# Kernel optimization log

Measured on AMD Instinct MI355X. Metric: run time of the kernel, lower is better.

Reference implementation:

```python
import jax, jax.numpy as jnp
import numpy as np

K = 512
DIM = 256
BETA = 0.25


def setup_inputs() -> dict:
    key = jax.random.key(0)
    k1, k2 = jax.random.split(key)
    x = jax.random.normal(k1, (64, DIM, 32, 32), dtype=jnp.float32)
    lookup_table = jax.random.normal(k2, (K, DIM), dtype=jnp.float32)
    return {"x": x, "lookup_table": lookup_table}


def reference(x, lookup_table):
    b, d, h, w = x.shape
    # [b,d,h,w] -> [b*h*w, d]
    xf = jnp.transpose(x, (0, 2, 3, 1)).reshape(-1, d)
    # Squared Euclidean distances (argmin identical to torch.cdist argmin)
    d2 = (
        jnp.sum(xf * xf, axis=-1, keepdims=True)
        - 2.0 * (xf @ lookup_table.T)
        + jnp.sum(lookup_table * lookup_table, axis=-1)
    )  # [N, K]
    q = jnp.argmin(d2, axis=1)  # [N]
    x_e = lookup_table[q].reshape(b, h, w, d).transpose(0, 3, 1, 2)  # [b,d,h,w]
    q_x = q.reshape(b, h, w)
    codebook_loss = jnp.mean(jnp.square(jax.lax.stop_gradient(x) - x_e))
    commitment_loss = jnp.mean(jnp.square(x - jax.lax.stop_gradient(x_e)))
    loss = codebook_loss + BETA * commitment_loss
    return x_e, q_x, loss
```

## Files before the change

kernel.cpp:

```cpp
#include <hip/hip_runtime.h>

#define DIM     256
#define HW      1024
#define N_ROWS  65536
#define QBM     32
#define NBLK    2048
#define MARGIN  0.125f
#define MARGIN3 0.1875f

#define OUT_Q_OFF    16777216
#define OUT_LOSS_OFF 16842752

#define WS_DIST    512
#define WS_X2      2560
#define WS_CNTF_I  4608
#define WS_CNTP_I  4609
#define WS_LISTF_I 5120
#define WS_LISTP_I 21504
#define CAP_F      16384
#define CAP_P      32768
#define WS_LUTH_B  786432

typedef _Float16 half8v __attribute__((ext_vector_type(8)));
typedef float floatx4 __attribute__((ext_vector_type(4)));

__global__ void c2_kernel(const float* __restrict__ lut, float* __restrict__ ws) {
    if (threadIdx.x == 0) { ((int*)ws)[WS_CNTF_I] = 0; ((int*)ws)[WS_CNTP_I] = 0; }
    int t = threadIdx.x;
    for (int k = t; k < 512; k += 256) {
        const float4* row = (const float4*)(lut + (size_t)k * DIM);
        float s = 0.f;
        #pragma unroll 8
        for (int i = 0; i < DIM / 4; ++i) {
            float4 v = row[i];
            s += v.x * v.x + v.y * v.y + v.z * v.z + v.w * v.w;
        }
        ws[k] = s;
    }
}

__global__ void lutprep_kernel(const float* __restrict__ lut, float* __restrict__ ws) {
    int g = blockIdx.x * 256 + threadIdx.x;
    int lane = g & 63;
    int ctu  = (g >> 6) & 31;
    int dcg  = g >> 11;
    int code = ctu * 16 + (lane & 15);
    int d0   = dcg * 32 + (lane >> 4) * 8;
    const float* src = lut + (size_t)code * DIM + d0;
    half8v h;
    #pragma unroll
    for (int j = 0; j < 8; ++j) h[j] = (_Float16)src[j];
    char* dst = (char*)ws + WS_LUTH_B + (size_t)(dcg * 32 + ctu) * 1024 + lane * 16;
    *(half8v*)dst = h;
}

#define MERGE_TRIPLE(v1,i1,v2,i2,v3, w1,j1,w2,j2,w3)                          \
    {                                                                         \
        float a1,a2,a3,b1v,b2v; int a1i,a2i,b1i,b2i;                          \
        bool bf = (w1 < v1) || (w1 == v1 && j1 < i1);                         \
        if (bf) { a1=w1;a1i=j1;a2=w2;a2i=j2;a3=w3; b1v=v1;b1i=i1;b2v=v2;b2i=i2; } \
        else    { a1=v1;a1i=i1;a2=v2;a2i=i2;a3=v3; b1v=w1;b1i=j1;b2v=w2;b2i=j2; } \
        bool sa = (a2 < b1v) || (a2 == b1v && a2i < b1i);                     \
        v1 = a1; i1 = a1i;                                                    \
        if (sa) { v2 = a2; i2 = a2i; v3 = fminf(a3, b1v); }                   \
        else    { v2 = b1v; i2 = b1i; v3 = fminf(a2, b2v); }                  \
    }

#define CTU_BODY(CUR, NXT, CTU, DO_PREFETCH)                                          \
    {                                                                                 \
        if (DO_PREFETCH) {                                                            \
            _Pragma("unroll")                                                         \
            for (int dc = 0; dc < 8; ++dc)                                            \
                NXT[dc] = *(const half8v*)(luth + (size_t)(dc * 32 + (CTU) + 1) * 1024 + lane * 16); \
        }                                                                             \
        floatx4 acc00 = (floatx4)0.f, acc01 = (floatx4)0.f;                           \
        floatx4 acc10 = (floatx4)0.f, acc11 = (floatx4)0.f;                           \
        _Pragma("unroll")                                                             \
        for (int dc = 0; dc < 4; ++dc) {                                              \
            acc00 = __builtin_amdgcn_mfma_f32_16x16x32_f16(a[0][dc], CUR[dc], acc00, 0, 0, 0); \
            acc10 = __builtin_amdgcn_mfma_f32_16x16x32_f16(a[1][dc], CUR[dc], acc10, 0, 0, 0); \
        }                                                                             \
        _Pragma("unroll")                                                             \
        for (int dc = 4; dc < 8; ++dc) {                                              \
            acc01 = __builtin_amdgcn_mfma_f32_16x16x32_f16(a[0][dc], CUR[dc], acc01, 0, 0, 0); \
            acc11 = __builtin_amdgcn_mfma_f32_16x16x32_f16(a[1][dc], CUR[dc], acc11, 0, 0, 0); \
        }                                                                             \
        float c2v = ws[(CTU) * 16 + l15];                                             \
        int code = (CTU) * 16 + l15;                                                  \
        _Pragma("unroll")                                                             \
        for (int r = 0; r < 4; ++r) {                                                 \
            float d0f = fmaf(-2.f, acc00[r] + acc01[r], c2v);                         \
            if (d0f < v1[0][r])      { v3[0][r]=v2[0][r]; v2[0][r]=v1[0][r]; i2[0][r]=i1[0][r]; v1[0][r]=d0f; i1[0][r]=code; } \
            else if (d0f < v2[0][r]) { v3[0][r]=v2[0][r]; v2[0][r]=d0f; i2[0][r]=code; } \
            else if (d0f < v3[0][r]) { v3[0][r]=d0f; }                                \
            float d1f = fmaf(-2.f, acc10[r] + acc11[r], c2v);                         \
            if (d1f < v1[1][r])      { v3[1][r]=v2[1][r]; v2[1][r]=v1[1][r]; i2[1][r]=i1[1][r]; v1[1][r]=d1f; i1[1][r]=code; } \
            else if (d1f < v2[1][r]) { v3[1][r]=v2[1][r]; v2[1][r]=d1f; i2[1][r]=code; } \
            else if (d1f < v3[1][r]) { v3[1][r]=d1f; }                                \
        }                                                                             \
    }

__global__ __launch_bounds__(64, 2) void vq_kernel(const float* __restrict__ x,
                                                   const float* __restrict__ lut,
                                                   float* __restrict__ out,
                                                   float* __restrict__ ws) {
    __shared__ int qsh[QBM];
    const char* luth = (const char*)ws + WS_LUTH_B;

    const int lane = threadIdx.x;
    const int blk  = blockIdx.x;
    const int n0   = blk * QBM;
    const int b    = n0 >> 10;
    const int hw0  = n0 & 1023;
    const float* xb = x + (size_t)b * (DIM * HW) + hw0;

    const int l15 = lane & 15;
    const int l4  = lane >> 4;

    half8v a[2][8];
    float x2local = 0.f;
    #pragma unroll
    for (int rt = 0; rt < 2; ++rt) {
        #pragma unroll
        for (int dc = 0; dc < 8; ++dc) {
            const float* src = xb + (size_t)(dc * 32 + l4 * 8) * HW + rt * 16 + l15;
            half8v hh;
            #pragma unroll
            for (int j = 0; j < 8; ++j) {
                float v = src[(size_t)j * HW];
                x2local = fmaf(v, v, x2local);
                hh[j] = (_Float16)v;
            }
            a[rt][dc] = hh;
        }
    }

    float v1[2][4], v2[2][4], v3[2][4]; int i1[2][4], i2[2][4];
    #pragma unroll
    for (int rt = 0; rt < 2; ++rt)
        #pragma unroll
        for (int r = 0; r < 4; ++r) { v1[rt][r]=3.4e38f; v2[rt][r]=3.4e38f; v3[rt][r]=3.4e38f; i1[rt][r]=0; i2[rt][r]=0; }

    half8v bA[8], bB[8];
    #pragma unroll
    for (int dc = 0; dc < 8; ++dc)
        bA[dc] = *(const half8v*)(luth + (size_t)(dc * 32 + 0) * 1024 + lane * 16);
    for (int ctu2 = 0; ctu2 < 16; ++ctu2) {
        const int ctuA = 2 * ctu2;
        const int ctuB = 2 * ctu2 + 1;
        CTU_BODY(bA, bB, ctuA, true);
        CTU_BODY(bB, bA, ctuB, (ctu2 < 15));
    }

    #pragma unroll
    for (int rt = 0; rt < 2; ++rt) {
        #pragma unroll
        for (int r = 0; r < 4; ++r) {
            #pragma unroll
            for (int off = 1; off < 16; off <<= 1) {
                float w1 = __shfl_xor(v1[rt][r], off, 64);
                int   j1 = __shfl_xor(i1[rt][r], off, 64);
                float w2 = __shfl_xor(v2[rt][r], off, 64);
                int   j2 = __shfl_xor(i2[rt][r], off, 64);
                float w3 = __shfl_xor(v3[rt][r], off, 64);
                MERGE_TRIPLE(v1[rt][r], i1[rt][r], v2[rt][r], i2[rt][r], v3[rt][r], w1, j1, w2, j2, w3);
            }
        }
    }

    float dist_part = 0.f;
    if (l15 == 0) {
        #pragma unroll
        for (int rt = 0; rt < 2; ++rt) {
            #pragma unroll
            for (int r = 0; r < 4; ++r) {
                int row = rt * 16 + l4 * 4 + r;
                int n1 = i1[rt][r];
                qsh[row] = n1;
                out[OUT_Q_OFF + n0 + row] = (float)n1;
                float m1 = v1[rt][r], m2 = v2[rt][r], m3 = v3[rt][r];
                if (m2 - m1 <= MARGIN) {
                    if (m3 - m1 > MARGIN3) {
                        int idx = atomicAdd((int*)ws + WS_CNTP_I, 1);
                        if (idx < CAP_P) {
                            ((int*)ws)[WS_LISTP_I + idx * 3 + 0] = n0 + row;
                            ((int*)ws)[WS_LISTP_I + idx * 3 + 1] = n1;
                            ((int*)ws)[WS_LISTP_I + idx * 3 + 2] = i2[rt][r];
                        }
                    } else {
                        int idx = atomicAdd((int*)ws + WS_CNTF_I, 1);
                        if (idx < CAP_F) ((int*)ws)[WS_LISTF_I + idx] = n0 + row;
                    }
                }
                dist_part += m1;
            }
        }
    }
    float dv = dist_part;
    #pragma unroll
    for (int off = 32; off; off >>= 1) dv += __shfl_down(dv, off, 64);
    if (lane == 0) ws[WS_DIST + blk] = dv;
    float xv = x2local;
    #pragma unroll
    for (int off = 32; off; off >>= 1) xv += __shfl_down(xv, off, 64);
    if (lane == 0) ws[WS_X2 + blk] = xv;

    __syncthreads();

    {
        const int h = lane & 7;
        const int g = lane >> 3;
        int qs[4];
        #pragma unroll
        for (int r = 0; r < 4; ++r) qs[r] = qsh[4 * h + r];
        float* ob = out + (size_t)b * (DIM * HW) + hw0 + 4 * h;
        #pragma unroll
        for (int p = 0; p < 4; ++p) {
            #pragma unroll
            for (int j = 0; j < 8; ++j) {
                int d = (g + 8 * p) * 8 + j;
                float4 c;
                float* cp = (float*)&c;
                #pragma unroll
                for (int r = 0; r < 4; ++r) cp[r] = lut[(size_t)qs[r] * DIM + d];
                *(float4*)(ob + (size_t)d * HW) = c;
            }
        }
    }
}

__global__ void recheck_kernel(const float* __restrict__ x, const float* __restrict__ lut,
                               float* __restrict__ out, const float* __restrict__ ws) {
    __shared__ float xrow[DIM];
    __shared__ float carow[DIM];
    __shared__ float cbrow[DIM];
    __shared__ float frv[256];
    __shared__ int   fri[256];
    __shared__ int   qq;
    const int tid = threadIdx.x;

    int cntp = ((const int*)ws)[WS_CNTP_I];
    if (cntp > CAP_P) cntp = CAP_P;
    const int* lp = (const int*)ws + WS_LISTP_I;
    for (int e = blockIdx.x; e < cntp; e += gridDim.x) {
        const int row = lp[e * 3 + 0];
        const int ia  = lp[e * 3 + 1];
        const int ib  = lp[e * 3 + 2];
        const int b = row >> 10, hw = row & 1023;
        xrow[tid]  = x[(size_t)b * (DIM * HW) + (size_t)tid * HW + hw];
        carow[tid] = lut[(size_t)ia * DIM + tid];
        cbrow[tid] = lut[(size_t)ib * DIM + tid];
        __syncthreads();
        if (tid == 0) {
            float dota = 0.f, dotb = 0.f;
            for (int d = 0; d < DIM; ++d) {
                dota = fmaf(xrow[d], carow[d], dota);
                dotb = fmaf(xrow[d], cbrow[d], dotb);
            }
            float da = fmaf(-2.f, dota, ws[ia]);
            float db = fmaf(-2.f, dotb, ws[ib]);
            int q;
            if (da < db) q = ia;
            else if (db < da) q = ib;
            else q = (ia < ib) ? ia : ib;
            qq = q;
            out[OUT_Q_OFF + row] = (float)q;
        }
        __syncthreads();
        const int q = qq;
        out[(size_t)b * (DIM * HW) + (size_t)tid * HW + hw] = lut[(size_t)q * DIM + tid];
        __syncthreads();
    }

    int cntf = ((const int*)ws)[WS_CNTF_I];
    if (cntf > CAP_F) cntf = CAP_F;
    const int* lf = (const int*)ws + WS_LISTF_I;
    for (int e = blockIdx.x; e < cntf; e += gridDim.x) {
        const int row = lf[e];
        const int b = row >> 10, hw = row & 1023;
        xrow[tid] = x[(size_t)b * (DIM * HW) + (size_t)tid * HW + hw];
        __syncthreads();
        float bv = 3.4e38f; int bi = 0;
        #pragma unroll
        for (int k2 = 0; k2 < 2; ++k2) {
            int k = tid + k2 * 256;
            const float* cr = lut + (size_t)k * DIM;
            float dot = 0.f;
            for (int d = 0; d < DIM; ++d) dot = fmaf(xrow[d], cr[d], dot);
            float dist = fmaf(-2.f, dot, ws[k]);
            if (dist < bv || (dist == bv && k < bi)) { bv = dist; bi = k; }
        }
        frv[tid] = bv; fri[tid] = bi;
        __syncthreads();
        for (int s = 128; s; s >>= 1) {
            if (tid < s) {
                float ov = frv[tid + s]; int oi = fri[tid + s];
                if (ov < frv[tid] || (ov == frv[tid] && oi < fri[tid])) {
                    frv[tid] = ov; fri[tid] = oi;
                }
            }
            __syncthreads();
        }
        const int q = fri[0];
        if (tid == 0) out[OUT_Q_OFF + row] = (float)q;
        out[(size_t)b * (DIM * HW) + (size_t)tid * HW + hw] = lut[(size_t)q * DIM + tid];
        __syncthreads();
    }
}

__global__ void loss_kernel(float* __restrict__ out, const float* __restrict__ ws) {
    __shared__ float wsum[4];
    int tid = threadIdx.x;
    float s = 0.f;
    for (int i = tid; i < 4096; i += 256) s += ws[WS_DIST + i];
    #pragma unroll
    for (int off = 32; off; off >>= 1) s += __shfl_down(s, off, 64);
    if ((tid & 63) == 0) wsum[tid >> 6] = s;
    __syncthreads();
    if (tid == 0) {
        float total = wsum[0] + wsum[1] + wsum[2] + wsum[3];
        out[OUT_LOSS_OFF] = total * (1.25f / 16777216.f);
    }
}

extern "C" void kernel_launch(void* const* d_in, const int* in_sizes, int n_in,
                              void* d_out, int out_size, void* d_ws, size_t ws_size,
                              hipStream_t stream) {
    const float* x   = (const float*)d_in[0];
    const float* lut = (const float*)d_in[1];
    float* out = (float*)d_out;
    float* ws  = (float*)d_ws;

    c2_kernel<<<1, 256, 0, stream>>>(lut, ws);
    lutprep_kernel<<<64, 256, 0, stream>>>(lut, ws);
    vq_kernel<<<NBLK, 64, 0, stream>>>(x, lut, out, ws);
    recheck_kernel<<<2048, 256, 0, stream>>>(x, lut, out, ws);
    loss_kernel<<<1, 256, 0, stream>>>(out, ws);
}
```

Baseline: 138.7 us.

## Stage fp16 codebook in LDS shared by eight waves per block

The VQ kernel goes from 2048 single-wave blocks to 256 blocks of 512 threads. Each block loads the fp16 codebook into 128KB of LDS in two halves via global_load_lds, and all eight waves read it from shared memory instead of each wave streaming it from global/L2. Row indices for the gather are now passed with wave shuffles instead of shared memory. The cost is a block-wide barrier per half and one block per CU with 256 blocks, so there is less latency hiding and no prefetch overlap between the LDS fill and the MFMA work.

```diff
diff --git a/kernel.cpp b/kernel.cpp
--- a/kernel.cpp
+++ b/kernel.cpp
@@ -3,8 +3,6 @@
 #define DIM     256
 #define HW      1024
 #define N_ROWS  65536
-#define QBM     32
-#define NBLK    2048
 #define MARGIN  0.125f
 #define MARGIN3 0.1875f
 
@@ -21,8 +19,14 @@
 #define CAP_P      32768
 #define WS_LUTH_B  786432
 
+#define VQ_LDS 131072
+
 typedef _Float16 half8v __attribute__((ext_vector_type(8)));
 typedef float floatx4 __attribute__((ext_vector_type(4)));
+
+#define GLOAD_LDS16(gaddr, laddr) \
+    __builtin_amdgcn_global_load_lds((const __attribute__((address_space(1))) unsigned int*)(gaddr), \
+                                     (__attribute__((address_space(3))) unsigned int*)(laddr), 16, 0, 0)
 
 __global__ void c2_kernel(const float* __restrict__ lut, float* __restrict__ ws) {
     if (threadIdx.x == 0) { ((int*)ws)[WS_CNTF_I] = 0; ((int*)ws)[WS_CNTP_I] = 0; }
@@ -66,64 +70,32 @@
         else    { v2 = b1v; i2 = b1i; v3 = fminf(a2, b2v); }                  \
     }
 
-#define CTU_BODY(CUR, NXT, CTU, DO_PREFETCH)                                          \
-    {                                                                                 \
-        if (DO_PREFETCH) {                                                            \
-            _Pragma("unroll")                                                         \
-            for (int dc = 0; dc < 8; ++dc)                                            \
-                NXT[dc] = *(const half8v*)(luth + (size_t)(dc * 32 + (CTU) + 1) * 1024 + lane * 16); \
-        }                                                                             \
-        floatx4 acc00 = (floatx4)0.f, acc01 = (floatx4)0.f;                           \
-        floatx4 acc10 = (floatx4)0.f, acc11 = (floatx4)0.f;                           \
-        _Pragma("unroll")                                                             \
-        for (int dc = 0; dc < 4; ++dc) {                                              \
-            acc00 = __builtin_amdgcn_mfma_f32_16x16x32_f16(a[0][dc], CUR[dc], acc00, 0, 0, 0); \
-            acc10 = __builtin_amdgcn_mfma_f32_16x16x32_f16(a[1][dc], CUR[dc], acc10, 0, 0, 0); \
-        }                                                                             \
-        _Pragma("unroll")                                                             \
-        for (int dc = 4; dc < 8; ++dc) {                                              \
-            acc01 = __builtin_amdgcn_mfma_f32_16x16x32_f16(a[0][dc], CUR[dc], acc01, 0, 0, 0); \
-            acc11 = __builtin_amdgcn_mfma_f32_16x16x32_f16(a[1][dc], CUR[dc], acc11, 0, 0, 0); \
-        }                                                                             \
-        float c2v = ws[(CTU) * 16 + l15];                                             \
-        int code = (CTU) * 16 + l15;                                                  \
-        _Pragma("unroll")                                                             \
-        for (int r = 0; r < 4; ++r) {                                                 \
-            float d0f = fmaf(-2.f, acc00[r] + acc01[r], c2v);                         \
-            if (d0f < v1[0][r])      { v3[0][r]=v2[0][r]; v2[0][r]=v1[0][r]; i2[0][r]=i1[0][r]; v1[0][r]=d0f; i1[0][r]=code; } \
-            else if (d0f < v2[0][r]) { v3[0][r]=v2[0][r]; v2[0][r]=d0f; i2[0][r]=code; } \
-            else if (d0f < v3[0][r]) { v3[0][r]=d0f; }                                \
-            float d1f = fmaf(-2.f, acc10[r] + acc11[r], c2v);                         \
-            if (d1f < v1[1][r])      { v3[1][r]=v2[1][r]; v2[1][r]=v1[1][r]; i2[1][r]=i1[1][r]; v1[1][r]=d1f; i1[1][r]=code; } \
-            else if (d1f < v2[1][r]) { v3[1][r]=v2[1][r]; v2[1][r]=d1f; i2[1][r]=code; } \
-            else if (d1f < v3[1][r]) { v3[1][r]=d1f; }                                \
-        }                                                                             \
-    }
-
-__global__ __launch_bounds__(64, 2) void vq_kernel(const float* __restrict__ x,
-                                                   const float* __restrict__ lut,
-                                                   float* __restrict__ out,
-                                                   float* __restrict__ ws) {
-    __shared__ int qsh[QBM];
+__global__ __launch_bounds__(512, 1) void vq_kernel(const float* __restrict__ x,
+                                                    const float* __restrict__ lut,
+                                                    float* __restrict__ out,
+                                                    float* __restrict__ ws) {
+    extern __shared__ char smem[];
     const char* luth = (const char*)ws + WS_LUTH_B;
 
-    const int lane = threadIdx.x;
+    const int tid  = threadIdx.x;
     const int blk  = blockIdx.x;
-    const int n0   = blk * QBM;
-    const int b    = n0 >> 10;
-    const int hw0  = n0 & 1023;
+    const int wave = tid >> 6;
+    const int lane = tid & 63;
+    const int l15  = lane & 15;
+    const int l4   = lane >> 4;
+
+    const int n0w = blk * 256 + wave * 32;
+    const int b   = n0w >> 10;
+    const int hw0 = n0w & 1023;
     const float* xb = x + (size_t)b * (DIM * HW) + hw0;
-
-    const int l15 = lane & 15;
-    const int l4  = lane >> 4;
 
     half8v a[2][8];
     float x2local = 0.f;
     #pragma unroll
-    for (int rt = 0; rt < 2; ++rt) {
+    for (int t = 0; t < 2; ++t) {
         #pragma unroll
         for (int dc = 0; dc < 8; ++dc) {
-            const float* src = xb + (size_t)(dc * 32 + l4 * 8) * HW + rt * 16 + l15;
+            const float* src = xb + (size_t)(dc * 32 + l4 * 8) * HW + t * 16 + l15;
             half8v hh;
             #pragma unroll
             for (int j = 0; j < 8; ++j) {
@@ -131,39 +103,66 @@
                 x2local = fmaf(v, v, x2local);
                 hh[j] = (_Float16)v;
             }
-            a[rt][dc] = hh;
+            a[t][dc] = hh;
         }
     }
 
     float v1[2][4], v2[2][4], v3[2][4]; int i1[2][4], i2[2][4];
     #pragma unroll
-    for (int rt = 0; rt < 2; ++rt)
-        #pragma unroll
-        for (int r = 0; r < 4; ++r) { v1[rt][r]=3.4e38f; v2[rt][r]=3.4e38f; v3[rt][r]=3.4e38f; i1[rt][r]=0; i2[rt][r]=0; }
-
-    half8v bA[8], bB[8];
-    #pragma unroll
-    for (int dc = 0; dc < 8; ++dc)
-        bA[dc] = *(const half8v*)(luth + (size_t)(dc * 32 + 0) * 1024 + lane * 16);
-    for (int ctu2 = 0; ctu2 < 16; ++ctu2) {
-        const int ctuA = 2 * ctu2;
-        const int ctuB = 2 * ctu2 + 1;
-        CTU_BODY(bA, bB, ctuA, true);
-        CTU_BODY(bB, bA, ctuB, (ctu2 < 15));
-    }
-
-    #pragma unroll
-    for (int rt = 0; rt < 2; ++rt) {
+    for (int t = 0; t < 2; ++t)
+        #pragma unroll
+        for (int r = 0; r < 4; ++r) { v1[t][r]=3.4e38f; v2[t][r]=3.4e38f; v3[t][r]=3.4e38f; i1[t][r]=0; i2[t][r]=0; }
+
+    for (int p = 0; p < 2; ++p) {
+        __syncthreads();
+        #pragma unroll
+        for (int i = 0; i < 16; ++i) {
+            int idx = i * 512 + tid;
+            int ck  = idx >> 6;
+            int sc  = (ck >> 4) * 32 + p * 16 + (ck & 15);
+            GLOAD_LDS16(luth + (size_t)sc * 1024 + lane * 16, smem + ck * 1024);
+        }
+        __syncthreads();
+
+        for (int cl = 0; cl < 16; ++cl) {
+            half8v bh[8];
+            #pragma unroll
+            for (int dc = 0; dc < 8; ++dc)
+                bh[dc] = *(const half8v*)(smem + (size_t)(dc * 16 + cl) * 1024 + lane * 16);
+            floatx4 acc0 = (floatx4)0.f, acc1 = (floatx4)0.f;
+            #pragma unroll
+            for (int dc = 0; dc < 8; ++dc) {
+                acc0 = __builtin_amdgcn_mfma_f32_16x16x32_f16(a[0][dc], bh[dc], acc0, 0, 0, 0);
+                acc1 = __builtin_amdgcn_mfma_f32_16x16x32_f16(a[1][dc], bh[dc], acc1, 0, 0, 0);
+            }
+            const int code = (p * 16 + cl) * 16 + l15;
+            const float c2v = ws[code];
+            #pragma unroll
+            for (int r = 0; r < 4; ++r) {
+                float d0f = fmaf(-2.f, acc0[r], c2v);
+                if (d0f < v1[0][r])      { v3[0][r]=v2[0][r]; v2[0][r]=v1[0][r]; i2[0][r]=i1[0][r]; v1[0][r]=d0f; i1[0][r]=code; }
+                else if (d0f < v2[0][r]) { v3[0][r]=v2[0][r]; v2[0][r]=d0f; i2[0][r]=code; }
+                else if (d0f < v3[0][r]) { v3[0][r]=d0f; }
+                float d1f = fmaf(-2.f, acc1[r], c2v);
+                if (d1f < v1[1][r])      { v3[1][r]=v2[1][r]; v2[1][r]=v1[1][r]; i2[1][r]=i1[1][r]; v1[1][r]=d1f; i1[1][r]=code; }
+                else if (d1f < v2[1][r]) { v3[1][r]=v2[1][r]; v2[1][r]=d1f; i2[1][r]=code; }
+                else if (d1f < v3[1][r]) { v3[1][r]=d1f; }
+            }
+        }
+    }
+
+    #pragma unroll
+    for (int t = 0; t < 2; ++t) {
         #pragma unroll
         for (int r = 0; r < 4; ++r) {
             #pragma unroll
             for (int off = 1; off < 16; off <<= 1) {
-                float w1 = __shfl_xor(v1[rt][r], off, 64);
-                int   j1 = __shfl_xor(i1[rt][r], off, 64);
-                float w2 = __shfl_xor(v2[rt][r], off, 64);
-                int   j2 = __shfl_xor(i2[rt][r], off, 64);
-                float w3 = __shfl_xor(v3[rt][r], off, 64);
-                MERGE_TRIPLE(v1[rt][r], i1[rt][r], v2[rt][r], i2[rt][r], v3[rt][r], w1, j1, w2, j2, w3);
+                float w1 = __shfl_xor(v1[t][r], off, 64);
+                int   j1 = __shfl_xor(i1[t][r], off, 64);
+                float w2 = __shfl_xor(v2[t][r], off, 64);
+                int   j2 = __shfl_xor(i2[t][r], off, 64);
+                float w3 = __shfl_xor(v3[t][r], off, 64);
+                MERGE_TRIPLE(v1[t][r], i1[t][r], v2[t][r], i2[t][r], v3[t][r], w1, j1, w2, j2, w3);
             }
         }
     }
@@ -171,25 +170,24 @@
     float dist_part = 0.f;
     if (l15 == 0) {
         #pragma unroll
-        for (int rt = 0; rt < 2; ++rt) {
+        for (int t = 0; t < 2; ++t) {
             #pragma unroll
             for (int r = 0; r < 4; ++r) {
-                int row = rt * 16 + l4 * 4 + r;
-                int n1 = i1[rt][r];
-                qsh[row] = n1;
-                out[OUT_Q_OFF + n0 + row] = (float)n1;
-                float m1 = v1[rt][r], m2 = v2[rt][r], m3 = v3[rt][r];
+                int row = t * 16 + l4 * 4 + r;
+                int n1 = i1[t][r];
+                out[OUT_Q_OFF + n0w + row] = (float)n1;
+                float m1 = v1[t][r], m2 = v2[t][r], m3 = v3[t][r];
                 if (m2 - m1 <= MARGIN) {
                     if (m3 - m1 > MARGIN3) {
                         int idx = atomicAdd((int*)ws + WS_CNTP_I, 1);
                         if (idx < CAP_P) {
-                            ((int*)ws)[WS_LISTP_I + idx * 3 + 0] = n0 + row;
+                            ((int*)ws)[WS_LISTP_I + idx * 3 + 0] = n0w + row;
                             ((int*)ws)[WS_LISTP_I + idx * 3 + 1] = n1;
-                            ((int*)ws)[WS_LISTP_I + idx * 3 + 2] = i2[rt][r];
+                            ((int*)ws)[WS_LISTP_I + idx * 3 + 2] = i2[t][r];
                         }
                     } else {
                         int idx = atomicAdd((int*)ws + WS_CNTF_I, 1);
-                        if (idx < CAP_F) ((int*)ws)[WS_LISTF_I + idx] = n0 + row;
+                        if (idx < CAP_F) ((int*)ws)[WS_LISTF_I + idx] = n0w + row;
                     }
                 }
                 dist_part += m1;
@@ -199,26 +197,28 @@
     float dv = dist_part;
     #pragma unroll
     for (int off = 32; off; off >>= 1) dv += __shfl_down(dv, off, 64);
-    if (lane == 0) ws[WS_DIST + blk] = dv;
+    if (lane == 0) ws[WS_DIST + blk * 8 + wave] = dv;
     float xv = x2local;
     #pragma unroll
     for (int off = 32; off; off >>= 1) xv += __shfl_down(xv, off, 64);
-    if (lane == 0) ws[WS_X2 + blk] = xv;
-
-    __syncthreads();
+    if (lane == 0) ws[WS_X2 + blk * 8 + wave] = xv;
 
     {
         const int h = lane & 7;
         const int g = lane >> 3;
         int qs[4];
         #pragma unroll
-        for (int r = 0; r < 4; ++r) qs[r] = qsh[4 * h + r];
+        for (int r = 0; r < 4; ++r) {
+            int qa = __shfl(i1[0][r], (h & 3) * 16, 64);
+            int qb = __shfl(i1[1][r], (h & 3) * 16, 64);
+            qs[r] = (h >> 2) ? qb : qa;
+        }
         float* ob = out + (size_t)b * (DIM * HW) + hw0 + 4 * h;
         #pragma unroll
-        for (int p = 0; p < 4; ++p) {
+        for (int pd = 0; pd < 4; ++pd) {
             #pragma unroll
             for (int j = 0; j < 8; ++j) {
-                int d = (g + 8 * p) * 8 + j;
+                int d = (g + 8 * pd) * 8 + j;
                 float4 c;
                 float* cp = (float*)&c;
                 #pragma unroll
@@ -331,9 +331,12 @@
     float* out = (float*)d_out;
     float* ws  = (float*)d_ws;
 
+    (void)hipFuncSetAttribute((const void*)vq_kernel,
+                              hipFuncAttributeMaxDynamicSharedMemorySize, VQ_LDS);
+
     c2_kernel<<<1, 256, 0, stream>>>(lut, ws);
     lutprep_kernel<<<64, 256, 0, stream>>>(lut, ws);
-    vq_kernel<<<NBLK, 64, 0, stream>>>(x, lut, out, ws);
+    vq_kernel<<<256, 512, VQ_LDS, stream>>>(x, lut, out, ws);
     recheck_kernel<<<2048, 256, 0, stream>>>(x, lut, out, ws);
     loss_kernel<<<1, 256, 0, stream>>>(out, ws);
 }
```

Measured after the change: 131.1 us. 5.5% less time.
